# Performance work log

Hardware: AMD Instinct MI355X
Metric: run time of the kernel (lower is better)

## Reference

```python
import jax, jax.numpy as jnp
import numpy as np


def setup_inputs() -> dict:
    key = jax.random.key(0)
    k1, k2, k3, k4 = jax.random.split(key, 4)
    B, S, C = 16, 2048, 512
    x = jax.random.normal(k1, (B, S, C), dtype=jnp.float32)
    x_prime = jax.random.normal(k2, (B, S, C), dtype=jnp.float32)
    W = jax.random.normal(k3, (C, C), dtype=jnp.float32) * (1.0 / np.sqrt(C))
    b = jax.random.normal(k4, (C,), dtype=jnp.float32) * 0.01
    return {"x": x, "x_prime": x_prime, "W": W, "b": b}


def reference(x, x_prime, W, b):
    # q = Linear(x_prime): [B, S, C]
    q = jnp.einsum("bsc,dc->bsd", x_prime, W) + b
    # score = tanh(x_prime) @ q^T : [B, S, S]
    score = jnp.einsum("bsc,btc->bst", jnp.tanh(x_prime), q)
    alpha = jax.nn.softmax(score, axis=-1)
    # y_att = alpha @ x : [B, S, C]
    y_att = jnp.einsum("bst,btc->bsc", alpha, x)
    # dropout is identity in eval mode
    return jnp.tanh(y_att)
```

## Files before the change

kernel.cpp:

```cpp
#include <hip/hip_runtime.h>
#include <hip/hip_bf16.h>
#include <math.h>

typedef __bf16 bf16x8 __attribute__((ext_vector_type(8)));
typedef float  f32x4  __attribute__((ext_vector_type(4)));

#define MFMA16(a, b, c) __builtin_amdgcn_mfma_f32_16x16x32_bf16((a), (b), (c), 0, 0, 0)

static constexpr int    kB  = 16;
static constexpr int    kS  = 2048;
static constexpr int    kC  = 512;
static constexpr size_t kNE = (size_t)kB * kS * kC;

static __device__ __forceinline__ void split_bf16(float v, __bf16 &hi, __bf16 &lo) {
  hi = (__bf16)v;
  lo = (__bf16)(v - (float)hi);
}

static __device__ __forceinline__ int swzb(int row, int e) {
  return ((row << 7) + (e << 1)) ^ ((row & 7) << 4);
}
static __device__ __forceinline__ int swzp(int row, int e) {
  return ((row << 8) + (e << 1)) ^ ((row & 7) << 4);
}

static __device__ __forceinline__ void split_store16_swz(
    float4 v0, float4 v1, float4 v2, float4 v3, char* hi, char* lo, int row, int e0) {
  float vv[16] = {v0.x, v0.y, v0.z, v0.w, v1.x, v1.y, v1.z, v1.w,
                  v2.x, v2.y, v2.z, v2.w, v3.x, v3.y, v3.z, v3.w};
  bf16x8 h0, h1, l0, l1;
#pragma unroll
  for (int i = 0; i < 8; ++i) {
    __bf16 a, b;
    split_bf16(vv[i], a, b);     h0[i] = a; l0[i] = b;
    split_bf16(vv[8 + i], a, b); h1[i] = a; l1[i] = b;
  }
  *(bf16x8*)(hi + swzb(row, e0))     = h0;
  *(bf16x8*)(hi + swzb(row, e0 + 8)) = h1;
  *(bf16x8*)(lo + swzb(row, e0))     = l0;
  *(bf16x8*)(lo + swzb(row, e0 + 8)) = l1;
}

__global__ __launch_bounds__(256) void k_tanh_split(
    const float* __restrict__ xp, __bf16* __restrict__ th, __bf16* __restrict__ tl) {
  size_t i = ((size_t)blockIdx.x * 256 + threadIdx.x) * 8;
  float4 a = *(const float4*)(xp + i);
  float4 b = *(const float4*)(xp + i + 4);
  float v[8] = {a.x, a.y, a.z, a.w, b.x, b.y, b.z, b.w};
  bf16x8 h, l;
#pragma unroll
  for (int k = 0; k < 8; ++k) {
    float t = tanhf(v[k]);
    __bf16 hh, ll;
    split_bf16(t, hh, ll);
    h[k] = hh; l[k] = ll;
  }
  *(bf16x8*)(th + i) = h;
  *(bf16x8*)(tl + i) = l;
}

__global__ __launch_bounds__(256) void k_transpose_x(
    const float* __restrict__ x, __bf16* __restrict__ xbt) {
  __shared__ float tile[64][65];
  int bid = blockIdx.x;
  int b   = bid >> 8;
  int t0  = ((bid >> 3) & 31) * 64;
  int c0  = (bid & 7) * 64;
  int row = threadIdx.x >> 2;
  int seg = threadIdx.x & 3;
  const float* src = x + (size_t)(b * kS + t0 + row) * kC + c0 + seg * 16;
  float4 v0 = *(const float4*)(src + 0);
  float4 v1 = *(const float4*)(src + 4);
  float4 v2 = *(const float4*)(src + 8);
  float4 v3 = *(const float4*)(src + 12);
  float vv[16] = {v0.x, v0.y, v0.z, v0.w, v1.x, v1.y, v1.z, v1.w,
                  v2.x, v2.y, v2.z, v2.w, v3.x, v3.y, v3.z, v3.w};
#pragma unroll
  for (int i = 0; i < 16; ++i) tile[row][seg * 16 + i] = vv[i];
  __syncthreads();
  bf16x8 o0, o1;
#pragma unroll
  for (int i = 0; i < 8; ++i) o0[i] = (__bf16)tile[seg * 16 + i][row];
#pragma unroll
  for (int i = 0; i < 8; ++i) o1[i] = (__bf16)tile[seg * 16 + 8 + i][row];
  __bf16* dst = xbt + (size_t)(b * kC + c0 + row) * kS + t0 + seg * 16;
  *(bf16x8*)(dst)     = o0;
  *(bf16x8*)(dst + 8) = o1;
}

__global__ __launch_bounds__(256) void k_qgemm(
    const float* __restrict__ xp, const float* __restrict__ W,
    const float* __restrict__ bias, __bf16* __restrict__ qh, __bf16* __restrict__ ql) {
  __shared__ __align__(16) char lds[32768];
  char* Ah = lds;
  char* Al = lds + 8192;
  char* Bh = lds + 16384;
  char* Bl = lds + 24576;

  int bid = blockIdx.x;
  int n0  = (bid & 7) * 64;
  int m0  = (bid >> 3) * 64;

  int tid  = threadIdx.x;
  int lane = tid & 63;
  int wave = tid >> 6;
  int qd   = lane >> 4;
  int cl   = lane & 15;
  int row  = tid >> 2;
  int seg  = tid & 3;

  f32x4 acc[4] = {};
  const float* srcA = xp + (size_t)(m0 + row) * kC + seg * 16;
  const float* srcB = W  + (size_t)(n0 + row) * kC + seg * 16;

  float4 va0, va1, va2, va3, vb0, vb1, vb2, vb3;
  auto load_ab = [&](int kc) {
    const float* a = srcA + kc * 64;
    va0 = *(const float4*)(a);      va1 = *(const float4*)(a + 4);
    va2 = *(const float4*)(a + 8);  va3 = *(const float4*)(a + 12);
    const float* bb = srcB + kc * 64;
    vb0 = *(const float4*)(bb);     vb1 = *(const float4*)(bb + 4);
    vb2 = *(const float4*)(bb + 8); vb3 = *(const float4*)(bb + 12);
  };

  load_ab(0);
  for (int kc = 0; kc < 8; ++kc) {
    split_store16_swz(va0, va1, va2, va3, Ah, Al, row, seg * 16);
    split_store16_swz(vb0, vb1, vb2, vb3, Bh, Bl, row, seg * 16);
    __syncthreads();
    if (kc < 7) load_ab(kc + 1);
    __builtin_amdgcn_s_setprio(1);
#pragma unroll
    for (int ks = 0; ks < 2; ++ks) {
      int ka = ks * 32 + qd * 8;
      bf16x8 ah = *(const bf16x8*)(Ah + swzb(wave * 16 + cl, ka));
      bf16x8 al = *(const bf16x8*)(Al + swzb(wave * 16 + cl, ka));
#pragma unroll
      for (int j = 0; j < 4; ++j) {
        bf16x8 bh = *(const bf16x8*)(Bh + swzb(j * 16 + cl, ka));
        bf16x8 bl = *(const bf16x8*)(Bl + swzb(j * 16 + cl, ka));
        acc[j] = MFMA16(ah, bh, acc[j]);
        acc[j] = MFMA16(ah, bl, acc[j]);
        acc[j] = MFMA16(al, bh, acc[j]);
      }
    }
    __builtin_amdgcn_s_setprio(0);
    __syncthreads();
  }
#pragma unroll
  for (int j = 0; j < 4; ++j) {
    int d = n0 + j * 16 + cl;
    float bv = bias[d];
#pragma unroll
    for (int r = 0; r < 4; ++r) {
      int m = m0 + wave * 16 + qd * 4 + r;
      float v = acc[j][r] + bv;
      __bf16 h, l;
      split_bf16(v, h, l);
      qh[(size_t)m * kC + d] = h;
      ql[(size_t)m * kC + d] = l;
    }
  }
}

__global__ __launch_bounds__(256, 2) void k_attn(
    const __bf16* __restrict__ th, const __bf16* __restrict__ tl,
    const __bf16* __restrict__ qh, const __bf16* __restrict__ ql,
    const __bf16* __restrict__ xbt, float* __restrict__ out) {
  __shared__ __align__(16) char lds[49152];
  char* Ah = lds;
  char* Al = lds + 8192;
  char* Bh = lds + 16384;
  char* Bl = lds + 32768;
  char* P  = lds;
  char* Xt = lds + 16384;

  int bid = blockIdx.x;
  int b   = (bid & 7) | ((bid >> 8) << 3);
  int s0  = ((bid >> 3) & 31) * 64;

  int tid  = threadIdx.x;
  int lane = tid & 63;
  int wave = tid >> 6;
  int qd   = lane >> 4;
  int cl   = lane & 15;

  const float LOG2E = 1.4426950408889634f;

  float m_r[4], l_r[4];
  f32x4 O[8][4] = {};
#pragma unroll
  for (int r = 0; r < 4; ++r) { m_r[r] = -INFINITY; l_r[r] = 0.f; }

  const size_t rowbase = (size_t)b * kS;

  const int arow = tid >> 2, aseg = tid & 3;
  const int brow = tid >> 1, bseg = tid & 1;
  const int xrow = tid >> 2, xseg = tid & 3;

  bf16x8 rah[2], ral[2], rbh[4], rbl[4], rx[4], pa[4];

  auto load_a = [&](int kc) {
    size_t g = (rowbase + s0 + arow) * kC + kc * 64 + aseg * 16;
    rah[0] = *(const bf16x8*)(th + g); rah[1] = *(const bf16x8*)(th + g + 8);
    ral[0] = *(const bf16x8*)(tl + g); ral[1] = *(const bf16x8*)(tl + g + 8);
  };
  auto load_b = [&](int kc, int t0q) {
    size_t g = (rowbase + t0q + brow) * kC + kc * 64 + bseg * 32;
#pragma unroll
    for (int u = 0; u < 4; ++u) {
      rbh[u] = *(const bf16x8*)(qh + g + u * 8);
      rbl[u] = *(const bf16x8*)(ql + g + u * 8);
    }
  };
  auto load_x = [&](int nc, int t0q) {
    size_t g = ((size_t)b * kC + nc * 64 + xrow) * kS + t0q + xseg * 32;
#pragma unroll
    for (int u = 0; u < 4; ++u) rx[u] = *(const bf16x8*)(xbt + g + u * 8);
  };

  load_a(0);
  load_b(0, 0);

  for (int tt = 0; tt < 16; ++tt) {
    int t0 = tt * 128;
    f32x4 Sacc[8] = {};
    for (int kc = 0; kc < 8; ++kc) {
      *(bf16x8*)(Ah + swzb(arow, aseg * 16))     = rah[0];
      *(bf16x8*)(Ah + swzb(arow, aseg * 16 + 8)) = rah[1];
      *(bf16x8*)(Al + swzb(arow, aseg * 16))     = ral[0];
      *(bf16x8*)(Al + swzb(arow, aseg * 16 + 8)) = ral[1];
#pragma unroll
      for (int u = 0; u < 4; ++u) {
        *(bf16x8*)(Bh + swzb(brow, bseg * 32 + u * 8)) = rbh[u];
        *(bf16x8*)(Bl + swzb(brow, bseg * 32 + u * 8)) = rbl[u];
      }
      __syncthreads();
      if (kc < 7) { load_a(kc + 1); load_b(kc + 1, t0); }
      __builtin_amdgcn_s_setprio(1);
#pragma unroll
      for (int ks = 0; ks < 2; ++ks) {
        int ka = ks * 32 + qd * 8;
        bf16x8 ah = *(const bf16x8*)(Ah + swzb(wave * 16 + cl, ka));
        bf16x8 al = *(const bf16x8*)(Al + swzb(wave * 16 + cl, ka));
#pragma unroll
        for (int j = 0; j < 8; ++j) {
          bf16x8 bh = *(const bf16x8*)(Bh + swzb(j * 16 + cl, ka));
          bf16x8 bl = *(const bf16x8*)(Bl + swzb(j * 16 + cl, ka));
          Sacc[j] = MFMA16(ah, bh, Sacc[j]);
          Sacc[j] = MFMA16(ah, bl, Sacc[j]);
          Sacc[j] = MFMA16(al, bh, Sacc[j]);
        }
      }
      __builtin_amdgcn_s_setprio(0);
      __syncthreads();
    }
    load_x(0, t0);
    float rmax[4];
#pragma unroll
    for (int r = 0; r < 4; ++r) {
      float v = Sacc[0][r];
#pragma unroll
      for (int j = 1; j < 8; ++j) v = fmaxf(v, Sacc[j][r]);
      rmax[r] = v;
    }
#pragma unroll
    for (int mk = 1; mk < 16; mk <<= 1)
#pragma unroll
      for (int r = 0; r < 4; ++r)
        rmax[r] = fmaxf(rmax[r], __shfl_xor(rmax[r], mk, 64));
    float alpha[4], rsum[4];
#pragma unroll
    for (int r = 0; r < 4; ++r) {
      float mn = fmaxf(m_r[r], rmax[r]);
      alpha[r] = exp2f((m_r[r] - mn) * LOG2E);
      m_r[r] = mn;
      rsum[r] = 0.f;
    }
#pragma unroll
    for (int j = 0; j < 8; ++j)
#pragma unroll
      for (int r = 0; r < 4; ++r) {
        float p = exp2f((Sacc[j][r] - m_r[r]) * LOG2E);
        Sacc[j][r] = p;
        rsum[r] += p;
      }
#pragma unroll
    for (int mk = 1; mk < 16; mk <<= 1)
#pragma unroll
      for (int r = 0; r < 4; ++r)
        rsum[r] += __shfl_xor(rsum[r], mk, 64);
    f32x4 av;
#pragma unroll
    for (int r = 0; r < 4; ++r) {
      l_r[r] = l_r[r] * alpha[r] + rsum[r];
      av[r] = alpha[r];
    }
#pragma unroll
    for (int nc = 0; nc < 8; ++nc)
#pragma unroll
      for (int nt = 0; nt < 4; ++nt)
        O[nc][nt] *= av;
#pragma unroll
    for (int j = 0; j < 8; ++j)
#pragma unroll
      for (int r = 0; r < 4; ++r) {
        int prow = wave * 16 + qd * 4 + r;
        int off  = ((prow << 8) + ((j * 16 + cl) << 1)) ^ ((prow & 7) << 4);
        *(__bf16*)(P + off) = (__bf16)Sacc[j][r];
      }
#pragma unroll
    for (int nc = 0; nc < 8; ++nc) {
#pragma unroll
      for (int u = 0; u < 4; ++u)
        *(bf16x8*)(Xt + swzp(xrow, xseg * 32 + u * 8)) = rx[u];
      __syncthreads();
      if (nc == 0) {
#pragma unroll
        for (int ks = 0; ks < 4; ++ks)
          pa[ks] = *(const bf16x8*)(P + swzp(wave * 16 + cl, ks * 32 + qd * 8));
      }
      if (nc < 7) {
        load_x(nc + 1, t0);
      } else if (tt < 15) {
        load_a(0);
        load_b(0, t0 + 128);
      }
      __builtin_amdgcn_s_setprio(1);
#pragma unroll
      for (int ks = 0; ks < 4; ++ks) {
        int ka = ks * 32 + qd * 8;
#pragma unroll
        for (int nt = 0; nt < 4; ++nt) {
          bf16x8 xb = *(const bf16x8*)(Xt + swzp(nt * 16 + cl, ka));
          O[nc][nt] = MFMA16(pa[ks], xb, O[nc][nt]);
        }
      }
      __builtin_amdgcn_s_setprio(0);
      __syncthreads();
    }
  }
#pragma unroll
  for (int r = 0; r < 4; ++r) {
    float inv = __builtin_amdgcn_rcpf(l_r[r]);
    size_t rowoff = (rowbase + s0 + wave * 16 + qd * 4 + r) * kC;
#pragma unroll
    for (int nc = 0; nc < 8; ++nc)
#pragma unroll
      for (int nt = 0; nt < 4; ++nt) {
        float v = O[nc][nt][r] * inv;
        float e = exp2f(2.f * LOG2E * v);
        out[rowoff + nc * 64 + nt * 16 + cl] = 1.f - 2.f * __builtin_amdgcn_rcpf(e + 1.f);
      }
  }
}

extern "C" void kernel_launch(void* const* d_in, const int* in_sizes, int n_in,
                              void* d_out, int out_size, void* d_ws, size_t ws_size,
                              hipStream_t stream) {
  const float* x    = (const float*)d_in[0];
  const float* xp   = (const float*)d_in[1];
  const float* W    = (const float*)d_in[2];
  const float* bias = (const float*)d_in[3];
  float* out = (float*)d_out;

  __bf16* ws  = (__bf16*)d_ws;
  __bf16* th  = ws;
  __bf16* tl  = ws + kNE;
  __bf16* qh  = ws + 2 * kNE;
  __bf16* ql  = ws + 3 * kNE;
  __bf16* xbt = ws + 4 * kNE;

  k_tanh_split<<<8192, 256, 0, stream>>>(xp, th, tl);
  k_transpose_x<<<4096, 256, 0, stream>>>(x, xbt);
  k_qgemm<<<4096, 256, 0, stream>>>(xp, W, bias, qh, ql);
  k_attn<<<512, 256, 0, stream>>>(th, tl, qh, ql, xbt, out);
}
```

Measured before the change: 1.069 ms.

## Use 32x32 MFMA tiles for PV product and drop register prefetch

```diff
diff --git a/kernel.cpp b/kernel.cpp
--- a/kernel.cpp
+++ b/kernel.cpp
@@ -4,8 +4,10 @@
 
 typedef __bf16 bf16x8 __attribute__((ext_vector_type(8)));
 typedef float  f32x4  __attribute__((ext_vector_type(4)));
+typedef float  f32x16 __attribute__((ext_vector_type(16)));
 
 #define MFMA16(a, b, c) __builtin_amdgcn_mfma_f32_16x16x32_bf16((a), (b), (c), 0, 0, 0)
+#define MFMA32(a, b, c) __builtin_amdgcn_mfma_f32_32x32x16_bf16((a), (b), (c), 0, 0, 0)
 
 static constexpr int    kB  = 16;
 static constexpr int    kS  = 2048;
@@ -167,13 +169,15 @@
     const __bf16* __restrict__ th, const __bf16* __restrict__ tl,
     const __bf16* __restrict__ qh, const __bf16* __restrict__ ql,
     const __bf16* __restrict__ xbt, float* __restrict__ out) {
-  __shared__ __align__(16) char lds[49152];
-  char* Ah = lds;
-  char* Al = lds + 8192;
-  char* Bh = lds + 16384;
-  char* Bl = lds + 32768;
-  char* P  = lds;
-  char* Xt = lds + 16384;
+  __shared__ __align__(16) char lds[49664];
+  char* Ah  = lds;
+  char* Al  = lds + 8192;
+  char* Bh  = lds + 16384;
+  char* Bl  = lds + 32768;
+  char* P   = lds;
+  char* Xt0 = lds + 16384;
+  char* Xt1 = lds + 32768;
+  float* stat = (float*)(lds + 49152);
 
   int bid = blockIdx.x;
   int b   = (bid & 7) | ((bid >> 8) << 3);
@@ -184,11 +188,15 @@
   int wave = tid >> 6;
   int qd   = lane >> 4;
   int cl   = lane & 15;
+  int l31  = lane & 31;
+  int lh   = lane >> 5;
+  int whalf = wave & 1;
+  int wcol  = wave >> 1;
 
   const float LOG2E = 1.4426950408889634f;
 
   float m_r[4], l_r[4];
-  f32x4 O[8][4] = {};
+  f32x16 O[8] = {};
 #pragma unroll
   for (int r = 0; r < 4; ++r) { m_r[r] = -INFINITY; l_r[r] = 0.f; }
 
@@ -197,46 +205,32 @@
   const int arow = tid >> 2, aseg = tid & 3;
   const int brow = tid >> 1, bseg = tid & 1;
   const int xrow = tid >> 2, xseg = tid & 3;
-
-  bf16x8 rah[2], ral[2], rbh[4], rbl[4], rx[4], pa[4];
-
-  auto load_a = [&](int kc) {
-    size_t g = (rowbase + s0 + arow) * kC + kc * 64 + aseg * 16;
-    rah[0] = *(const bf16x8*)(th + g); rah[1] = *(const bf16x8*)(th + g + 8);
-    ral[0] = *(const bf16x8*)(tl + g); ral[1] = *(const bf16x8*)(tl + g + 8);
-  };
-  auto load_b = [&](int kc, int t0q) {
-    size_t g = (rowbase + t0q + brow) * kC + kc * 64 + bseg * 32;
-#pragma unroll
-    for (int u = 0; u < 4; ++u) {
-      rbh[u] = *(const bf16x8*)(qh + g + u * 8);
-      rbl[u] = *(const bf16x8*)(ql + g + u * 8);
-    }
-  };
-  auto load_x = [&](int nc, int t0q) {
-    size_t g = ((size_t)b * kC + nc * 64 + xrow) * kS + t0q + xseg * 32;
-#pragma unroll
-    for (int u = 0; u < 4; ++u) rx[u] = *(const bf16x8*)(xbt + g + u * 8);
-  };
-
-  load_a(0);
-  load_b(0, 0);
+  const int prow = whalf * 32 + l31;
 
   for (int tt = 0; tt < 16; ++tt) {
     int t0 = tt * 128;
     f32x4 Sacc[8] = {};
     for (int kc = 0; kc < 8; ++kc) {
-      *(bf16x8*)(Ah + swzb(arow, aseg * 16))     = rah[0];
-      *(bf16x8*)(Ah + swzb(arow, aseg * 16 + 8)) = rah[1];
-      *(bf16x8*)(Al + swzb(arow, aseg * 16))     = ral[0];
-      *(bf16x8*)(Al + swzb(arow, aseg * 16 + 8)) = ral[1];
-#pragma unroll
-      for (int u = 0; u < 4; ++u) {
-        *(bf16x8*)(Bh + swzb(brow, bseg * 32 + u * 8)) = rbh[u];
-        *(bf16x8*)(Bl + swzb(brow, bseg * 32 + u * 8)) = rbl[u];
+      {
+        size_t g = (rowbase + s0 + arow) * kC + kc * 64 + aseg * 16;
+        bf16x8 h0 = *(const bf16x8*)(th + g), h1 = *(const bf16x8*)(th + g + 8);
+        bf16x8 l0 = *(const bf16x8*)(tl + g), l1 = *(const bf16x8*)(tl + g + 8);
+        *(bf16x8*)(Ah + swzb(arow, aseg * 16))     = h0;
+        *(bf16x8*)(Ah + swzb(arow, aseg * 16 + 8)) = h1;
+        *(bf16x8*)(Al + swzb(arow, aseg * 16))     = l0;
+        *(bf16x8*)(Al + swzb(arow, aseg * 16 + 8)) = l1;
+      }
+      {
+        size_t g = (rowbase + t0 + brow) * kC + kc * 64 + bseg * 32;
+#pragma unroll
+        for (int u = 0; u < 4; ++u) {
+          bf16x8 vh = *(const bf16x8*)(qh + g + u * 8);
+          bf16x8 vl = *(const bf16x8*)(ql + g + u * 8);
+          *(bf16x8*)(Bh + swzb(brow, bseg * 32 + u * 8)) = vh;
+          *(bf16x8*)(Bl + swzb(brow, bseg * 32 + u * 8)) = vl;
+        }
       }
       __syncthreads();
-      if (kc < 7) { load_a(kc + 1); load_b(kc + 1, t0); }
       __builtin_amdgcn_s_setprio(1);
 #pragma unroll
       for (int ks = 0; ks < 2; ++ks) {
@@ -255,7 +249,6 @@
       __builtin_amdgcn_s_setprio(0);
       __syncthreads();
     }
-    load_x(0, t0);
     float rmax[4];
 #pragma unroll
     for (int r = 0; r < 4; ++r) {
@@ -290,68 +283,81 @@
 #pragma unroll
       for (int r = 0; r < 4; ++r)
         rsum[r] += __shfl_xor(rsum[r], mk, 64);
-    f32x4 av;
-#pragma unroll
-    for (int r = 0; r < 4; ++r) {
+#pragma unroll
+    for (int r = 0; r < 4; ++r)
       l_r[r] = l_r[r] * alpha[r] + rsum[r];
-      av[r] = alpha[r];
-    }
-#pragma unroll
-    for (int nc = 0; nc < 8; ++nc)
-#pragma unroll
-      for (int nt = 0; nt < 4; ++nt)
-        O[nc][nt] *= av;
+    if (cl == 0) {
+#pragma unroll
+      for (int r = 0; r < 4; ++r) stat[wave * 16 + qd * 4 + r] = alpha[r];
+    }
 #pragma unroll
     for (int j = 0; j < 8; ++j)
 #pragma unroll
       for (int r = 0; r < 4; ++r) {
-        int prow = wave * 16 + qd * 4 + r;
-        int off  = ((prow << 8) + ((j * 16 + cl) << 1)) ^ ((prow & 7) << 4);
-        *(__bf16*)(P + off) = (__bf16)Sacc[j][r];
-      }
-#pragma unroll
-    for (int nc = 0; nc < 8; ++nc) {
-#pragma unroll
-      for (int u = 0; u < 4; ++u)
-        *(bf16x8*)(Xt + swzp(xrow, xseg * 32 + u * 8)) = rx[u];
+        int pr = wave * 16 + qd * 4 + r;
+        *(__bf16*)(P + swzp(pr, j * 16 + cl)) = (__bf16)Sacc[j][r];
+      }
+    __syncthreads();
+    float ar[16];
+#pragma unroll
+    for (int i = 0; i < 16; ++i)
+      ar[i] = stat[whalf * 32 + (i & 3) + 8 * (i >> 2) + 4 * lh];
+    bf16x8 pa[8];
+#pragma unroll
+    for (int ks = 0; ks < 8; ++ks)
+      pa[ks] = *(const bf16x8*)(P + swzp(prow, ks * 16 + lh * 8));
+#pragma unroll
+    for (int t = 0; t < 8; ++t)
+#pragma unroll
+      for (int i = 0; i < 16; ++i)
+        O[t][i] *= ar[i];
+#pragma unroll
+    for (int step = 0; step < 4; ++step) {
+      {
+        size_t g0 = ((size_t)b * kC + step * 64 + xrow) * kS + t0 + xseg * 32;
+        size_t g1 = g0 + (size_t)256 * kS;
+#pragma unroll
+        for (int u = 0; u < 4; ++u)
+          *(bf16x8*)(Xt0 + swzp(xrow, xseg * 32 + u * 8)) = *(const bf16x8*)(xbt + g0 + u * 8);
+#pragma unroll
+        for (int u = 0; u < 4; ++u)
+          *(bf16x8*)(Xt1 + swzp(xrow, xseg * 32 + u * 8)) = *(const bf16x8*)(xbt + g1 + u * 8);
+      }
       __syncthreads();
-      if (nc == 0) {
-#pragma unroll
-        for (int ks = 0; ks < 4; ++ks)
-          pa[ks] = *(const bf16x8*)(P + swzp(wave * 16 + cl, ks * 32 + qd * 8));
-      }
-      if (nc < 7) {
-        load_x(nc + 1, t0);
-      } else if (tt < 15) {
-        load_a(0);
-        load_b(0, t0 + 128);
-      }
+      const char* Xt = wcol ? Xt1 : Xt0;
       __builtin_amdgcn_s_setprio(1);
 #pragma unroll
-      for (int ks = 0; ks < 4; ++ks) {
-        int ka = ks * 32 + qd * 8;
-#pragma unroll
-        for (int nt = 0; nt < 4; ++nt) {
-          bf16x8 xb = *(const bf16x8*)(Xt + swzp(nt * 16 + cl, ka));
-          O[nc][nt] = MFMA16(pa[ks], xb, O[nc][nt]);
+      for (int ks = 0; ks < 8; ++ks) {
+#pragma unroll
+        for (int nloc = 0; nloc < 2; ++nloc) {
+          bf16x8 xb = *(const bf16x8*)(Xt + swzp(nloc * 32 + l31, ks * 16 + lh * 8));
+          O[step * 2 + nloc] = MFMA32(pa[ks], xb, O[step * 2 + nloc]);
         }
       }
       __builtin_amdgcn_s_setprio(0);
       __syncthreads();
     }
   }
-#pragma unroll
-  for (int r = 0; r < 4; ++r) {
-    float inv = __builtin_amdgcn_rcpf(l_r[r]);
-    size_t rowoff = (rowbase + s0 + wave * 16 + qd * 4 + r) * kC;
-#pragma unroll
-    for (int nc = 0; nc < 8; ++nc)
-#pragma unroll
-      for (int nt = 0; nt < 4; ++nt) {
-        float v = O[nc][nt][r] * inv;
-        float e = exp2f(2.f * LOG2E * v);
-        out[rowoff + nc * 64 + nt * 16 + cl] = 1.f - 2.f * __builtin_amdgcn_rcpf(e + 1.f);
-      }
+  if (cl == 0) {
+#pragma unroll
+    for (int r = 0; r < 4; ++r) stat[wave * 16 + qd * 4 + r] = l_r[r];
+  }
+  __syncthreads();
+  float linv[16];
+#pragma unroll
+  for (int i = 0; i < 16; ++i)
+    linv[i] = __builtin_amdgcn_rcpf(stat[whalf * 32 + (i & 3) + 8 * (i >> 2) + 4 * lh]);
+#pragma unroll
+  for (int t = 0; t < 8; ++t) {
+    int colbase = wcol * 256 + (t >> 1) * 64 + (t & 1) * 32 + l31;
+#pragma unroll
+    for (int i = 0; i < 16; ++i) {
+      int rowl = (i & 3) + 8 * (i >> 2) + 4 * lh;
+      float v = O[t][i] * linv[i];
+      float e = exp2f(2.f * LOG2E * v);
+      out[(rowbase + s0 + whalf * 32 + rowl) * kC + colbase] =
+          1.f - 2.f * __builtin_amdgcn_rcpf(e + 1.f);
+    }
   }
 }
 
```

After: 1.090 ms. Within noise of the previous version (+1.9%).
